# Performance work log

Measured on AMD Instinct MI355X. Metric: run time of the kernel, lower is better.

## Reference

```python
import jax, jax.numpy as jnp
import numpy as np
from jax import lax

B, D, H, W = 1, 16, 128, 128
CIN, NPTS = 16, 100000
NEG = np.float32(-1e30)  # stands in for -inf at unoccupied voxels in max pooling


def _conv(x, wk):
    # Minkowski stride-1 conv at occupied sites == dense zero-padded conv masked to occupancy
    return lax.conv_general_dilated(x, wk, (1, 1, 1), 'SAME',
                                    dimension_numbers=('NCDHW', 'OIDHW', 'NCDHW'))


def _crelu(x, wk, occ):
    return jnp.where(occ, jax.nn.relu(_conv(x, wk)), 0.0)


def _mpool(x, occ, spatial):
    # Minkowski max pool: max over occupied voxels in the kernel window; output coords are
    # the stride-floored input coords (z halved). spatial=True -> kernel (3,3,3) else (3,1,1).
    xm = jnp.where(occ, x, NEG)
    win = (1, 1, 3, 3, 3) if spatial else (1, 1, 3, 1, 1)
    pad = [(0, 0), (0, 0), (1, 1), (1, 1), (1, 1)] if spatial else [(0, 0), (0, 0), (1, 1), (0, 0), (0, 0)]
    y = lax.reduce_window(xm, NEG, lax.max, win, (1, 1, 2, 1, 1), pad)
    occ2 = occ[:, :, 0::2] | occ[:, :, 1::2]
    return jnp.where(occ2, y, 0.0), occ2


def _forward(voxel_features, coors, ws, batch_size):
    b, d, h, w = coors[:, 0], coors[:, 1], coors[:, 2], coors[:, 3]
    cin = voxel_features.shape[1]
    grid = jnp.zeros((batch_size, D, H, W, cin), voxel_features.dtype).at[b, d, h, w].set(voxel_features)
    x = jnp.transpose(grid, (0, 4, 1, 2, 3))  # (B, C, D, H, W)
    occ = jnp.zeros((batch_size, 1, D, H, W), bool).at[b, 0, d, h, w].set(True)

    x = _crelu(x, ws[0], occ)
    x = _crelu(x, ws[1], occ)
    x, occ = _mpool(x, occ, True)
    for wk in ws[2:5]:
        x = _crelu(x, wk, occ)
    x, occ = _mpool(x, occ, True)
    for wk in ws[5:8]:
        x = _crelu(x, wk, occ)
    x, occ = _mpool(x, occ, False)  # kernel (3,1,1)
    n, c, dd, hh, ww = x.shape  # (B, 64, 2, H, W)
    return x.reshape(n, c * dd, hh, ww)


def setup_inputs():
    key = jax.random.key(0)
    ks = jax.random.split(key, 9)
    rng = np.random.default_rng(0)
    lin = rng.permutation(D * H * W)[:NPTS].astype(np.int64)  # unique occupied voxels
    d = (lin // (H * W)).astype(np.int32)
    h = ((lin // W) % H).astype(np.int32)
    w = (lin % W).astype(np.int32)
    coors = jnp.asarray(np.stack([np.zeros(NPTS, np.int32), d, h, w], axis=1))
    vf = jax.random.normal(ks[0], (NPTS, CIN), jnp.float32)

    def cw(k, o, i):
        return jax.random.normal(k, (o, i, 3, 3, 3), jnp.float32) * np.float32(1.0 / np.sqrt(i * 27))

    chans = [(32, CIN), (64, 32)] + [(64, 64)] * 6
    ws = {f"w{j + 1}": cw(ks[j + 1], o, i) for j, (o, i) in enumerate(chans)}
    return dict(voxel_features=vf, coors=coors, batch_size=B, **ws)


def reference(voxel_features, coors, batch_size, w1, w2, w3, w4, w5, w6, w7, w8):
    return _forward(voxel_features, coors, (w1, w2, w3, w4, w5, w6, w7, w8), batch_size)
```

## Files before the change

kernel.cpp:

```cpp
#include <hip/hip_runtime.h>
#include <stdint.h>

#define DEV __device__ __forceinline__

typedef float f32x4 __attribute__((ext_vector_type(4)));
typedef short s16x8 __attribute__((ext_vector_type(8)));
typedef unsigned int u32x4 __attribute__((ext_vector_type(4)));
typedef unsigned int u32x2 __attribute__((ext_vector_type(2)));

static constexpr int HM = 128, WM = 128;
static constexpr int HP = 130, WP = 130;

DEV unsigned short f2bf(float f) {
  unsigned int u = __float_as_uint(f);
  return (unsigned short)((u + 0x7fffu + ((u >> 16) & 1u)) >> 16);
}
DEV float bf2f(unsigned short s) { return __uint_as_float(((unsigned int)s) << 16); }

DEV void gll16(const void* g, void* l) {
  __builtin_amdgcn_global_load_lds((const unsigned int*)g, (unsigned int*)l, 16, 0, 0);
}
DEV void waitvmc(int n) {
  if (n == 0)      asm volatile("s_waitcnt vmcnt(0)" ::: "memory");
  else if (n == 1) asm volatile("s_waitcnt vmcnt(1)" ::: "memory");
  else if (n == 2) asm volatile("s_waitcnt vmcnt(2)" ::: "memory");
  else if (n == 3) asm volatile("s_waitcnt vmcnt(3)" ::: "memory");
  else if (n == 4) asm volatile("s_waitcnt vmcnt(4)" ::: "memory");
  else if (n == 5) asm volatile("s_waitcnt vmcnt(5)" ::: "memory");
  else if (n == 7) asm volatile("s_waitcnt vmcnt(7)" ::: "memory");
  else             asm volatile("s_waitcnt vmcnt(0)" ::: "memory");
}

__global__ __launch_bounds__(256)
void scatter_k(const float* __restrict__ vf, const int* __restrict__ co,
               unsigned short* __restrict__ x,
               unsigned char* __restrict__ o0, unsigned char* __restrict__ o1,
               unsigned char* __restrict__ o2, unsigned char* __restrict__ o3,
               int npts) {
  int i = blockIdx.x * 256 + threadIdx.x;
  if (i >= npts) return;
  int d = co[i * 4 + 1], h = co[i * 4 + 2], w = co[i * 4 + 3];
  unsigned short* dst = x + (size_t)(((d + 1) * HP + (h + 1)) * WP + (w + 1)) * 32;
#pragma unroll
  for (int c = 0; c < 16; ++c) dst[c] = f2bf(vf[i * 16 + c]);
  int hw = h * WM + w;
  o0[d * (HM * WM) + hw] = 1;
  o1[(d >> 1) * (HM * WM) + hw] = 1;
  o2[(d >> 2) * (HM * WM) + hw] = 1;
  o3[(d >> 3) * (HM * WM) + hw] = 1;
}

__global__ __launch_bounds__(256)
void wcvt_all_k(const float* s0, const float* s1, const float* s2, const float* s3,
                const float* s4, const float* s5, const float* s6, const float* s7,
                unsigned short* __restrict__ dst) {
  int t = blockIdx.x * 256 + threadIdx.x;
  const int CIs[8] = {16, 32, 64, 64, 64, 64, 64, 64};
  const int CId[8] = {32, 32, 64, 64, 64, 64, 64, 64};
  const int COa[8] = {32, 64, 64, 64, 64, 64, 64, 64};
  const float* srcs[8] = {s0, s1, s2, s3, s4, s5, s6, s7};
  int start = 0;
#pragma unroll
  for (int i = 0; i < 8; ++i) {
    int sz = 27 * COa[i] * CId[i];
    if (t >= start && t < start + sz) {
      int l = t - start;
      int ci = l % CId[i];
      int r = l / CId[i];
      int cco = r % COa[i];
      int tap = r / COa[i];
      float v = (ci < CIs[i]) ? srcs[i][(cco * CIs[i] + ci) * 27 + tap] : 0.0f;
      dst[t] = f2bf(v);
    }
    start += sz;
  }
}

template <int CI, int CO, int ROWS>
__global__ __launch_bounds__(512, 4)
void conv_k(const unsigned short* __restrict__ xin, unsigned short* __restrict__ xout,
            const unsigned short* __restrict__ wt, const unsigned char* __restrict__ occ,
            int D) {
  constexpr int SLOTS = CI / 8;
  constexpr int MSK = SLOTS - 1;
  constexpr int CIB = CI / 32;
  constexpr int NM = CO / 16;
  constexpr int J = ROWS;
  constexpr int XROWS = ROWS + 2;
  constexpr int RXI = (128 * SLOTS) / 512;
  constexpr int NCW = 3 * CO * SLOTS;
  constexpr int KW = (NCW + 511) / 512;
  constexpr int NA = 2 * RXI + KW;
  constexpr int NB = RXI + KW;
  constexpr int WOFF = 3 * CO * CI;
  __shared__ __align__(16) unsigned short xs[XROWS * 130 * CI];
  __shared__ __align__(16) unsigned short wls[2 * WOFF];

  int nb = gridDim.x;
  int bid = blockIdx.x;
  int blk = (bid & 7) * (nb >> 3) + (bid >> 3);
  int tid = threadIdx.x;
  constexpr int HBLK = 128 / ROWS;
  int d = blk / HBLK, hb = blk - (blk / HBLK) * HBLK;
  int h0 = hb * ROWS;
  int lane = tid & 63, wv = tid >> 6, ln = lane & 15, lg = lane >> 4;

  auto issueX = [&](int kd, int ri) {
#pragma unroll
    for (int i = 0; i < RXI; ++i) {
      int c = i * 512 + tid;
      int vcol = 1 + c / SLOTS;
      int sl = c - (c / SLOTS) * SLOTS;
      int v = ri * 130 + vcol;
      int ss = sl ^ (v & MSK);
      const unsigned short* g =
          xin + ((size_t)((d + kd) * HP + (h0 + ri)) * WP + vcol) * CI + ss * 8;
      gll16(g, xs + (size_t)(ri * 130 + 1) * CI + (size_t)c * 8);
    }
  };
  auto issueW = [&](int kd, int kh, unsigned short* wbuf) {
#pragma unroll
    for (int i = 0; i < KW; ++i) {
      int c = i * 512 + tid;
      if (c >= NCW) c -= NCW;
      int u = c / SLOTS, sl = c - (c / SLOTS) * SLOTS;
      int kw = u / CO, cc = u - kw * CO;
      int ss = sl ^ (u & MSK);
      const unsigned short* g =
          wt + ((size_t)((kd * 3 + kh) * 3 + kw) * CO + cc) * CI + ss * 8;
      gll16(g, wbuf + (size_t)c * 8);
    }
  };

  {
    constexpr int CH8 = CO / 8;
    int hv = 2 * HP * WP + D * (2 * WP + 2 * HM);
    int tot8 = hv * CH8;
    int per = (tot8 + nb - 1) / nb;
    int base = blk * per, lim = base + per;
    if (lim > tot8) lim = tot8;
    for (int c = base + tid; c < lim; c += 512) {
      int i = c / CH8, sub = c - (c / CH8) * CH8;
      int p, hh, ww;
      if (i < 2 * HP * WP) {
        p = (i >= HP * WP) ? (D + 1) : 0;
        int rem = i - ((i >= HP * WP) ? HP * WP : 0);
        hh = rem / WP; ww = rem - hh * WP;
      } else {
        constexpr int PH = 2 * WP + 2 * HM;
        int j2 = i - 2 * HP * WP;
        p = j2 / PH + 1;
        int r2 = j2 - (p - 1) * PH;
        if (r2 < 2 * WP) { hh = (r2 >= WP) ? (HP - 1) : 0; ww = r2 % WP; }
        else { int r3 = r2 - 2 * WP; hh = 1 + (r3 & 127); ww = (r3 < HM) ? 0 : (WP - 1); }
      }
      *(u32x4*)(xout + ((size_t)(p * HP + hh) * WP + ww) * CO + sub * 8) = (u32x4)0u;
    }
  }
  issueX(0, 0);
  issueX(0, 1);
  issueW(0, 0, wls);
  for (int t = tid; t < XROWS * 2 * SLOTS; t += 512) {
    int ri = t / (2 * SLOTS);
    int r2 = t - ri * 2 * SLOTS;
    int colv = (r2 >= SLOTS) ? 129 : 0;
    int sl = r2 & MSK;
    *(u32x4*)(xs + (size_t)(ri * 130 + colv) * CI + sl * 8) = (u32x4)0u;
  }
  float on[J];
#pragma unroll
  for (int j = 0; j < J; ++j) {
    int vox = wv * (16 * J) + j * 16 + ln;
    on[j] = occ[(d * HM + (h0 + (vox >> 7))) * WM + (vox & 127)] ? 1.0f : 0.0f;
  }
  asm volatile("s_waitcnt lgkmcnt(0)" ::: "memory");

  f32x4 acc[NM][J];
#pragma unroll
  for (int m = 0; m < NM; ++m)
#pragma unroll
    for (int j = 0; j < J; ++j) acc[m][j] = (f32x4)0.0f;

#pragma unroll
  for (int s = 0; s < 9; ++s) {
    int kd = s / 3, kh = s - 3 * kd;
    unsigned short* wnext = wls + ((s + 1) & 1) * WOFF;
    if (kh == 0) {
#pragma unroll
      for (int ri = 2; ri < XROWS; ++ri) issueX(kd, ri);
      issueW(kd, 1, wnext);
    } else if (kh == 1) {
      if (kd < 2) issueX(kd + 1, 0);
      issueW(kd, 2, wnext);
    } else {
      if (kd < 2) {
        issueX(kd + 1, 1);
        issueW(kd + 1, 0, wnext);
      }
    }
    __builtin_amdgcn_sched_barrier(0);
    if (kh == 0)      waitvmc(NA);
    else if (kh == 1) waitvmc(kd < 2 ? NB : KW);
    else              waitvmc(kd < 2 ? NB : 0);
    __builtin_amdgcn_sched_barrier(0);
    __builtin_amdgcn_s_barrier();
    __builtin_amdgcn_sched_barrier(0);
    const unsigned short* wc = wls + (s & 1) * WOFF;
    __builtin_amdgcn_s_setprio(1);
#pragma unroll
    for (int kw = 0; kw < 3; ++kw) {
#pragma unroll
      for (int cb = 0; cb < CIB; ++cb) {
        int slot = cb * 4 + lg;
        s16x8 a[NM], b[J];
#pragma unroll
        for (int m = 0; m < NM; ++m) {
          int u = kw * CO + m * 16 + ln;
          a[m] = *(const s16x8*)(wc + ((size_t)u * SLOTS + (slot ^ (u & MSK))) * 8);
        }
#pragma unroll
        for (int j = 0; j < J; ++j) {
          int vox = wv * (16 * J) + j * 16 + ln;
          int v = ((vox >> 7) + kh) * 130 + (vox & 127) + kw;
          b[j] = *(const s16x8*)(xs + ((size_t)v * SLOTS + (slot ^ (v & MSK))) * 8);
        }
#pragma unroll
        for (int m = 0; m < NM; ++m)
#pragma unroll
          for (int j = 0; j < J; ++j)
            acc[m][j] = __builtin_amdgcn_mfma_f32_16x16x32_bf16(a[m], b[j], acc[m][j], 0, 0, 0);
      }
    }
    __builtin_amdgcn_s_setprio(0);
    __builtin_amdgcn_sched_barrier(0);
    if (s < 8) __builtin_amdgcn_s_barrier();
  }

#pragma unroll
  for (int j = 0; j < J; ++j) {
    int vox = wv * (16 * J) + j * 16 + ln;
    int r = vox >> 7, w2 = vox & 127;
    unsigned short* dst = xout + ((size_t)((d + 1) * HP + (h0 + r + 1)) * WP + (w2 + 1)) * CO;
#pragma unroll
    for (int m = 0; m < NM; ++m) {
      unsigned short q0 = f2bf(fmaxf(acc[m][j][0], 0.0f) * on[j]);
      unsigned short q1 = f2bf(fmaxf(acc[m][j][1], 0.0f) * on[j]);
      unsigned short q2 = f2bf(fmaxf(acc[m][j][2], 0.0f) * on[j]);
      unsigned short q3 = f2bf(fmaxf(acc[m][j][3], 0.0f) * on[j]);
      u32x2 pv;
      pv.x = (unsigned int)q0 | ((unsigned int)q1 << 16);
      pv.y = (unsigned int)q2 | ((unsigned int)q3 << 16);
      *(u32x2*)&dst[m * 16 + lg * 4] = pv;
    }
  }
}

template <int C, int ROWS>
__global__ __launch_bounds__(256)
void pool_sp_k(const unsigned short* __restrict__ xin, unsigned short* __restrict__ xout,
               const unsigned char* __restrict__ oc, int Dout) {
  constexpr int CH = C / 8;
  constexpr int WR = ROWS + 2;
  __shared__ __align__(16) unsigned short dm[WR * 66 * C];
  int nb = gridDim.x;
  int bid = blockIdx.x;
  int blk = (bid & 7) * (nb >> 3) + (bid >> 3);
  int tid = threadIdx.x;
  constexpr int HT = 128 / ROWS;
  int wh = blk & 1;
  int rest = blk >> 1;
  int ht = rest % HT, dp = rest / HT;
  int h0 = ht * ROWS;
  int w0 = wh * 64;

  {
    int hv = 2 * HP * WP + Dout * 2 * WP;
    int tot8 = hv * CH;
    int per = (tot8 + nb - 1) / nb;
    int base = blk * per, lim = base + per;
    if (lim > tot8) lim = tot8;
    for (int c = base + tid; c < lim; c += 256) {
      int i = c / CH, sub = c - (c / CH) * CH;
      int p, hh, ww;
      if (i < 2 * HP * WP) {
        p = (i >= HP * WP) ? (Dout + 1) : 0;
        int rem = i - ((i >= HP * WP) ? HP * WP : 0);
        hh = rem / WP; ww = rem - hh * WP;
      } else {
        int j2 = i - 2 * HP * WP;
        p = j2 / (2 * WP) + 1;
        int r2 = j2 - (p - 1) * (2 * WP);
        hh = (r2 >= WP) ? (HP - 1) : 0;
        ww = r2 % WP;
      }
      *(u32x4*)(xout + ((size_t)(p * HP + hh) * WP + ww) * C + sub * 8) = (u32x4)0u;
    }
  }

  for (int idx = tid; idx < WR * 66 * CH; idx += 256) {
    int ri = idx / (66 * CH);
    int rem = idx - ri * (66 * CH);
    int wc = rem / CH, c8 = rem - wc * CH;
    float mx[8];
#pragma unroll
    for (int q = 0; q < 8; ++q) mx[q] = 0.0f;
#pragma unroll
    for (int dd = 0; dd < 3; ++dd) {
      const unsigned short* p =
          xin + ((size_t)((2 * dp + dd) * HP + (h0 + ri)) * WP + (w0 + wc)) * C + c8 * 8;
      u32x4 v = *(const u32x4*)p;
      const unsigned short* u = (const unsigned short*)&v;
#pragma unroll
      for (int q = 0; q < 8; ++q) mx[q] = fmaxf(mx[q], bf2f(u[q]));
    }
    unsigned short o[8];
#pragma unroll
    for (int q = 0; q < 8; ++q) o[q] = f2bf(mx[q]);
    *(u32x4*)&dm[(size_t)(ri * 66 + wc) * C + c8 * 8] = *(const u32x4*)o;
  }
  __syncthreads();

  for (int idx = tid; idx < ROWS * 64 * CH; idx += 256) {
    int r = idx / (64 * CH);
    int rem = idx - r * (64 * CH);
    int wc2 = rem / CH, c8 = rem - wc2 * CH;
    float mx[8];
#pragma unroll
    for (int q = 0; q < 8; ++q) mx[q] = 0.0f;
#pragma unroll
    for (int rr = 0; rr < 3; ++rr)
#pragma unroll
      for (int ww = 0; ww < 3; ++ww) {
        u32x4 v = *(const u32x4*)&dm[(size_t)((r + rr) * 66 + (wc2 + ww)) * C + c8 * 8];
        const unsigned short* u = (const unsigned short*)&v;
#pragma unroll
        for (int q = 0; q < 8; ++q) mx[q] = fmaxf(mx[q], bf2f(u[q]));
      }
    bool onv = oc[(dp * HM + (h0 + r)) * WM + (w0 + wc2)] != 0;
    unsigned short o[8];
#pragma unroll
    for (int q = 0; q < 8; ++q) o[q] = onv ? f2bf(mx[q]) : (unsigned short)0;
    *(u32x4*)(xout + ((size_t)((dp + 1) * HP + (h0 + r + 1)) * WP + (w0 + wc2 + 1)) * C +
              c8 * 8) = *(const u32x4*)o;
  }
}

__global__ __launch_bounds__(256)
void pool_d_k(const unsigned short* __restrict__ xin, float* __restrict__ out,
              const unsigned char* __restrict__ oc) {
  int t = blockIdx.x * 256 + threadIdx.x;
  int c8 = t & 7, w = (t >> 3) & 127, h = (t >> 10) & 127, dp = (t >> 17) & 1;
  float mx[8];
#pragma unroll
  for (int q = 0; q < 8; ++q) mx[q] = 0.0f;
#pragma unroll
  for (int dd = 0; dd < 3; ++dd) {
    const unsigned short* p =
        xin + ((size_t)((2 * dp + dd) * HP + (h + 1)) * WP + (w + 1)) * 64 + c8 * 8;
    u32x4 v = *(const u32x4*)p;
    const unsigned short* u = (const unsigned short*)&v;
#pragma unroll
    for (int q = 0; q < 8; ++q) mx[q] = fmaxf(mx[q], bf2f(u[q]));
  }
  bool on = oc[(dp * HM + h) * WM + w] != 0;
#pragma unroll
  for (int q = 0; q < 8; ++q) {
    int c = c8 * 8 + q;
    out[((c * 2 + dp) * HM + h) * WM + w] = on ? mx[q] : 0.0f;
  }
}

extern "C" void kernel_launch(void* const* d_in, const int* in_sizes, int n_in,
                              void* d_out, int out_size, void* d_ws, size_t ws_size,
                              hipStream_t stream) {
  (void)n_in; (void)out_size; (void)ws_size;
  const float* vf = (const float*)d_in[0];
  const int* co = (const int*)d_in[1];
  int npts = in_sizes[1] / 4;

  char* ws = (char*)d_ws;
  const size_t SA = (size_t)18 * 130 * 130 * 64 * 2;
  const size_t SB = (size_t)10 * 130 * 130 * 64 * 2;
  unsigned short* P = (unsigned short*)ws;
  unsigned short* Q = (unsigned short*)(ws + SA);
  unsigned short* R = P;
  unsigned char* occ0 = (unsigned char*)(ws + SA + SB);
  unsigned char* occ1 = occ0 + 16 * HM * WM;
  unsigned char* occ2 = occ1 + 8 * HM * WM;
  unsigned char* occ3 = occ2 + 4 * HM * WM;
  unsigned short* wb[8];
  {
    unsigned short* p = (unsigned short*)(occ3 + 2 * HM * WM);
    const int wsz[8] = {27 * 32 * 32, 27 * 64 * 32, 27 * 64 * 64, 27 * 64 * 64,
                        27 * 64 * 64, 27 * 64 * 64, 27 * 64 * 64, 27 * 64 * 64};
    for (int i = 0; i < 8; ++i) { wb[i] = p; p += wsz[i]; }
  }

  hipMemsetAsync(R, 0, (size_t)18 * 130 * 130 * 32 * 2, stream);
  hipMemsetAsync(occ0, 0, (size_t)(16 + 8 + 4 + 2) * HM * WM, stream);

  scatter_k<<<(npts + 255) / 256, 256, 0, stream>>>(vf, co, R, occ0, occ1, occ2, occ3, npts);

  {
    int tot = 27 * (32 * 32 + 64 * 32 + 6 * 64 * 64);
    wcvt_all_k<<<tot / 256, 256, 0, stream>>>(
        (const float*)d_in[3], (const float*)d_in[4], (const float*)d_in[5],
        (const float*)d_in[6], (const float*)d_in[7], (const float*)d_in[8],
        (const float*)d_in[9], (const float*)d_in[10], wb[0]);
  }

  conv_k<32, 32, 4><<<16 * 32, 512, 0, stream>>>(R, Q, wb[0], occ0, 16);
  conv_k<32, 64, 4><<<16 * 32, 512, 0, stream>>>(Q, P, wb[1], occ0, 16);
  pool_sp_k<64, 4><<<8 * 32 * 2, 256, 0, stream>>>(P, Q, occ1, 8);
  conv_k<64, 64, 4><<<8 * 32, 512, 0, stream>>>(Q, P, wb[2], occ1, 8);
  conv_k<64, 64, 4><<<8 * 32, 512, 0, stream>>>(P, Q, wb[3], occ1, 8);
  conv_k<64, 64, 4><<<8 * 32, 512, 0, stream>>>(Q, P, wb[4], occ1, 8);
  pool_sp_k<64, 2><<<4 * 64 * 2, 256, 0, stream>>>(P, Q, occ2, 4);
  conv_k<64, 64, 2><<<4 * 64, 512, 0, stream>>>(Q, P, wb[5], occ2, 4);
  conv_k<64, 64, 2><<<4 * 64, 512, 0, stream>>>(P, Q, wb[6], occ2, 4);
  conv_k<64, 64, 2><<<4 * 64, 512, 0, stream>>>(Q, P, wb[7], occ2, 4);
  pool_d_k<<<(2 * 128 * 128 * 8) / 256, 256, 0, stream>>>(P, (float*)d_out, occ3);
}
```

Before: 263.4 us.

## Load conv weights directly into registers instead of double-buffered LDS

Weights are repacked into a per-lane fragment layout (taps x CI-blocks x CO x 32) so each lane can load its MFMA A-operands straight from global memory into registers for every kd/kh step. This removes the LDS weight double buffer, its async copies and wait counts, and the LDS reads of weights in the inner loop. It frees shared memory and LDS bandwidth at the cost of more VGPRs, so launch bounds are lowered from 4 to 2 blocks per CU. Weight global loads sit on the critical path each step, which may expose latency.

```diff
diff --git a/kernel.cpp b/kernel.cpp
--- a/kernel.cpp
+++ b/kernel.cpp
@@ -65,10 +65,14 @@
     int sz = 27 * COa[i] * CId[i];
     if (t >= start && t < start + sz) {
       int l = t - start;
-      int ci = l % CId[i];
-      int r = l / CId[i];
+      int k32 = l & 31;
+      int r = l >> 5;
       int cco = r % COa[i];
-      int tap = r / COa[i];
+      int r2 = r / COa[i];
+      int cib = CId[i] / 32;
+      int cb = r2 % cib;
+      int tap = r2 / cib;
+      int ci = cb * 32 + k32;
       float v = (ci < CIs[i]) ? srcs[i][(cco * CIs[i] + ci) * 27 + tap] : 0.0f;
       dst[t] = f2bf(v);
     }
@@ -77,7 +81,7 @@
 }
 
 template <int CI, int CO, int ROWS>
-__global__ __launch_bounds__(512, 4)
+__global__ __launch_bounds__(512, 2)
 void conv_k(const unsigned short* __restrict__ xin, unsigned short* __restrict__ xout,
             const unsigned short* __restrict__ wt, const unsigned char* __restrict__ occ,
             int D) {
@@ -88,13 +92,7 @@
   constexpr int J = ROWS;
   constexpr int XROWS = ROWS + 2;
   constexpr int RXI = (128 * SLOTS) / 512;
-  constexpr int NCW = 3 * CO * SLOTS;
-  constexpr int KW = (NCW + 511) / 512;
-  constexpr int NA = 2 * RXI + KW;
-  constexpr int NB = RXI + KW;
-  constexpr int WOFF = 3 * CO * CI;
   __shared__ __align__(16) unsigned short xs[XROWS * 130 * CI];
-  __shared__ __align__(16) unsigned short wls[2 * WOFF];
 
   int nb = gridDim.x;
   int bid = blockIdx.x;
@@ -116,19 +114,6 @@
       const unsigned short* g =
           xin + ((size_t)((d + kd) * HP + (h0 + ri)) * WP + vcol) * CI + ss * 8;
       gll16(g, xs + (size_t)(ri * 130 + 1) * CI + (size_t)c * 8);
-    }
-  };
-  auto issueW = [&](int kd, int kh, unsigned short* wbuf) {
-#pragma unroll
-    for (int i = 0; i < KW; ++i) {
-      int c = i * 512 + tid;
-      if (c >= NCW) c -= NCW;
-      int u = c / SLOTS, sl = c - (c / SLOTS) * SLOTS;
-      int kw = u / CO, cc = u - kw * CO;
-      int ss = sl ^ (u & MSK);
-      const unsigned short* g =
-          wt + ((size_t)((kd * 3 + kh) * 3 + kw) * CO + cc) * CI + ss * 8;
-      gll16(g, wbuf + (size_t)c * 8);
     }
   };
 
@@ -159,7 +144,6 @@
   }
   issueX(0, 0);
   issueX(0, 1);
-  issueW(0, 0, wls);
   for (int t = tid; t < XROWS * 2 * SLOTS; t += 512) {
     int ri = t / (2 * SLOTS);
     int r2 = t - ri * 2 * SLOTS;
@@ -184,40 +168,39 @@
 #pragma unroll
   for (int s = 0; s < 9; ++s) {
     int kd = s / 3, kh = s - 3 * kd;
-    unsigned short* wnext = wls + ((s + 1) & 1) * WOFF;
+    s16x8 wa[3][CIB][NM];
+#pragma unroll
+    for (int kw = 0; kw < 3; ++kw)
+#pragma unroll
+      for (int cb = 0; cb < CIB; ++cb)
+#pragma unroll
+        for (int m = 0; m < NM; ++m)
+          wa[kw][cb][m] = *(const s16x8*)(
+              wt + (((size_t)(((kd * 3 + kh) * 3 + kw) * CIB + cb)) * CO + (m * 16 + ln)) * 32 +
+              lg * 8);
+    __builtin_amdgcn_sched_barrier(0);
     if (kh == 0) {
 #pragma unroll
       for (int ri = 2; ri < XROWS; ++ri) issueX(kd, ri);
-      issueW(kd, 1, wnext);
     } else if (kh == 1) {
       if (kd < 2) issueX(kd + 1, 0);
-      issueW(kd, 2, wnext);
     } else {
-      if (kd < 2) {
-        issueX(kd + 1, 1);
-        issueW(kd + 1, 0, wnext);
-      }
+      if (kd < 2) issueX(kd + 1, 1);
     }
     __builtin_amdgcn_sched_barrier(0);
-    if (kh == 0)      waitvmc(NA);
-    else if (kh == 1) waitvmc(kd < 2 ? NB : KW);
-    else              waitvmc(kd < 2 ? NB : 0);
+    if (kh == 0)      waitvmc(2 * RXI);
+    else if (kd < 2)  waitvmc(RXI);
+    else              waitvmc(0);
     __builtin_amdgcn_sched_barrier(0);
     __builtin_amdgcn_s_barrier();
     __builtin_amdgcn_sched_barrier(0);
-    const unsigned short* wc = wls + (s & 1) * WOFF;
     __builtin_amdgcn_s_setprio(1);
 #pragma unroll
     for (int kw = 0; kw < 3; ++kw) {
 #pragma unroll
       for (int cb = 0; cb < CIB; ++cb) {
         int slot = cb * 4 + lg;
-        s16x8 a[NM], b[J];
-#pragma unroll
-        for (int m = 0; m < NM; ++m) {
-          int u = kw * CO + m * 16 + ln;
-          a[m] = *(const s16x8*)(wc + ((size_t)u * SLOTS + (slot ^ (u & MSK))) * 8);
-        }
+        s16x8 b[J];
 #pragma unroll
         for (int j = 0; j < J; ++j) {
           int vox = wv * (16 * J) + j * 16 + ln;
@@ -228,7 +211,8 @@
         for (int m = 0; m < NM; ++m)
 #pragma unroll
           for (int j = 0; j < J; ++j)
-            acc[m][j] = __builtin_amdgcn_mfma_f32_16x16x32_bf16(a[m], b[j], acc[m][j], 0, 0, 0);
+            acc[m][j] =
+                __builtin_amdgcn_mfma_f32_16x16x32_bf16(wa[kw][cb][m], b[j], acc[m][j], 0, 0, 0);
       }
     }
     __builtin_amdgcn_s_setprio(0);
```

Result: slower. 403.1 us (+53.0%).
